# Optimization experiments

Measured on AMD Instinct MI355X. Metric: run time of the kernel, lower is better.

## Reference

```python
import jax, jax.numpy as jnp
import numpy as np

# static sizes (see shape_source)
IN_SIZE = 50000
M = 3            # n_modalities
N0 = 40960       # layer-0 sampled source nodes
N1 = 16384       # layer-0 dst == layer-1 src
B = 4096         # batch (final dst nodes)
HEADS = 4
DIM = 64
HD = HEADS * DIM # 256, integration_size
DEG0, DEG1 = 16, 16
E0, E1 = N1 * DEG0, B * DEG1
NEG_SLOPE = 0.2  # GATConv default negative_slope


def gat_conv(x_src, e_src, e_dst, n_dst, W, att, bias):
    """PyG GATConv with bipartite input (x, None): attention uses only alpha_l.
    x_src: [Ns, HD]; W: [HD, HD]; att: [1, H, C]; returns [n_dst, HD]."""
    x_l = (x_src @ W.T).reshape(-1, HEADS, DIM)            # [Ns, H, C]
    alpha_l = (x_l * att).sum(-1)                          # [Ns, H]
    logits = jax.nn.leaky_relu(alpha_l[e_src], NEG_SLOPE)  # [E, H]
    m = jax.ops.segment_max(logits, e_dst, num_segments=n_dst)
    m = jnp.where(jnp.isfinite(m), m, 0.0)                 # guard empty segments
    e = jnp.exp(logits - m[e_dst])
    denom = jax.ops.segment_sum(e, e_dst, num_segments=n_dst)
    a = e / (denom[e_dst] + 1e-16)                         # edge softmax per dst
    msg = x_l[e_src] * a[:, :, None]                       # [E, H, C]
    out = jax.ops.segment_sum(msg, e_dst, num_segments=n_dst)
    return out.reshape(n_dst, HD) + bias


def interp(scales_param, mask, key):
    """Interp module, evaluate=False, idxs = range(M)."""
    scales = jax.nn.softmax(scales_param, axis=-1)         # [1, M]
    rm = jax.random.randint(key, mask.shape, 0, 2).astype(jnp.float32)
    rm = rm + (1.0 / (1.0 + rm.sum(-1)) ** 20)[:, None]
    rm = rm + (1.0 / (mask.sum(-1) ** 20))[:, None]
    rm = jax.lax.stop_gradient(jnp.floor(rm))              # .int().float()
    rm = rm / (rm + 1e-10)
    m = mask * rm
    m = jax.nn.softmax(m + (1.0 - m) * (-1e10), axis=-1)   # [B, M]
    return scales, m


def setup_inputs() -> dict:
    key = jax.random.key(0)
    ks = jax.random.split(key, 12)
    s = 0.05
    return {
        "masks": jnp.ones((B, M), jnp.float32),
        "n_ids": jax.random.randint(ks[0], (M, N0), 0, IN_SIZE, dtype=jnp.int32),
        "e0_src": jax.random.randint(ks[1], (M, E0), 0, N0, dtype=jnp.int32),
        "e0_dst": jnp.repeat(jnp.arange(N1, dtype=jnp.int32), DEG0),
        "e1_src": jax.random.randint(ks[2], (M, E1), 0, N1, dtype=jnp.int32),
        "e1_dst": jnp.repeat(jnp.arange(B, dtype=jnp.int32), DEG1),
        "pre_W": jax.random.normal(ks[3], (M, HD, IN_SIZE), jnp.float32) * s,
        "pre_b": jax.random.normal(ks[4], (M, HD), jnp.float32) * s,
        "gat_W": jax.random.normal(ks[5], (M, HD, HD), jnp.float32) * s,
        "gat_att": jax.random.normal(ks[6], (M, 1, HEADS, DIM), jnp.float32) * s,
        "gat_b": jax.random.normal(ks[7], (M, HD), jnp.float32) * s,
        "scales_param": jnp.full((1, M), 1.0 / M, jnp.float32),
        "emb_W": jax.random.normal(ks[8], (128, HD), jnp.float32) * s,
        "emb_b": jax.random.normal(ks[9], (128,), jnp.float32) * s,
    }


def reference(masks, n_ids, e0_src, e0_dst, e1_src, e1_dst,
              pre_W, pre_b, gat_W, gat_att, gat_b,
              scales_param, emb_W, emb_b):
    scales, interp_masks = interp(scales_param, masks, jax.random.key(42))
    x_mod = jnp.zeros((B, HD), dtype=masks.dtype)
    for i in range(M):  # small fixed modality loop (structurally distinct params)
        # one-hot(n_id) @ W.T + b  ==  gather of columns of W (same math)
        x = jnp.take(pre_W[i], n_ids[i], axis=1).T + pre_b[i]        # [N0, HD]
        g0 = gat_conv(x, e0_src[i], e0_dst, N1, gat_W[i], gat_att[i], gat_b[i])
        g1 = gat_conv(g0, e1_src[i], e1_dst, B, gat_W[i], gat_att[i], gat_b[i])
        # x_store_layer = [g0[:B] (sliced), g0[:B] (x_pre), g1]; x = sum + g1
        xm = 2.0 * g0[:B] + 2.0 * g1                                  # [B, HD]
        xm = scales[:, i] * interp_masks[:, i].reshape(-1, 1) * xm
        x_mod = x_mod + xm
    emb = x_mod @ emb_W.T + emb_b                                     # [B, 128]
    dot = emb @ emb.T                                                 # [B, B]
    return dot, emb, scales
```

## Files before the change

kernel.cpp:

```cpp
#include <hip/hip_runtime.h>
#include <hip/hip_bf16.h>
#include <cstdint>

#define IN_SZ 50000
#define PADC  50048
#define NM 3
#define N0 40960
#define N1 16384
#define NB 4096
#define HD 256
#define DEG 16
#define E0 (N1*DEG)
#define E1 (NB*DEG)

using short8v = __attribute__((ext_vector_type(8))) short;
using floatx4 = __attribute__((ext_vector_type(4))) float;
typedef unsigned short ushort_t;

__device__ __forceinline__ ushort_t f2bf(float f){
  uint32_t u = __float_as_uint(f);
  uint32_t r = u + 0x7FFFu + ((u>>16)&1u);
  return (ushort_t)(r>>16);
}
__device__ __forceinline__ float bf2f(ushort_t h){
  return __uint_as_float(((uint32_t)h)<<16);
}
__device__ __forceinline__ void gload_lds16(const void* g, void* l){
  __builtin_amdgcn_global_load_lds(
      (const __attribute__((address_space(1))) void*)g,
      (__attribute__((address_space(3))) void*)l, 16, 0, 0);
}

__device__ __forceinline__ uint32_t rotl32(uint32_t x, uint32_t d){ return (x<<d)|(x>>(32u-d)); }

__device__ void tf2x32(uint32_t k0, uint32_t k1, uint32_t c0, uint32_t c1,
                       uint32_t& y0, uint32_t& y1)
{
  uint32_t ks2 = k0 ^ k1 ^ 0x1BD11BDAu;
  uint32_t x0 = c0 + k0, x1 = c1 + k1;
#define R4(a,b,c,d) \
  x0+=x1; x1=rotl32(x1,a); x1^=x0; \
  x0+=x1; x1=rotl32(x1,b); x1^=x0; \
  x0+=x1; x1=rotl32(x1,c); x1^=x0; \
  x0+=x1; x1=rotl32(x1,d); x1^=x0;
  R4(13,15,26,6)  x0+=k1;  x1+=ks2+1u;
  R4(17,29,16,24) x0+=ks2; x1+=k0+2u;
  R4(13,15,26,6)  x0+=k0;  x1+=k1+3u;
  R4(17,29,16,24) x0+=k1;  x1+=ks2+4u;
  R4(13,15,26,6)  x0+=ks2; x1+=k0+5u;
#undef R4
  y0=x0; y1=x1;
}

__global__ __launch_bounds__(256) void prep_k(
    const float* __restrict__ masks, const float* __restrict__ sp,
    float* __restrict__ coef, float* __restrict__ scales_out,
    const float* __restrict__ emb_W, float* __restrict__ wT,
    const float* __restrict__ gat_W, ushort_t* __restrict__ gWhi, ushort_t* __restrict__ gWlo,
    const float* __restrict__ pre_b, const float* __restrict__ gat_att,
    const float* __restrict__ gat_b, float* __restrict__ bsum, float* __restrict__ batt,
    float* __restrict__ watt)
{
  int blk = blockIdx.x;
  int t = threadIdx.x;
  if (blk < 16){
    int b = blk*256 + t;
    float s0=sp[0], s1=sp[1], s2=sp[2];
    float mx = fmaxf(s0,fmaxf(s1,s2));
    float e0=expf(s0-mx), e1=expf(s1-mx), e2=expf(s2-mx);
    float inv = 1.f/(e0+e1+e2);
    float sc[3] = {e0*inv, e1*inv, e2*inv};
    if (b == 0){ scales_out[0]=sc[0]; scales_out[1]=sc[1]; scales_out[2]=sc[2]; }
    uint32_t bits[3];
    uint32_t K0,K1, t0,t1;
    tf2x32(0u,42u,0u,1u,K0,K1);
    for (int i=0;i<3;i++){
      uint32_t idx = (uint32_t)(b*3+i);
      tf2x32(K0,K1,0u,idx,t0,t1);
      bits[i] = (t0 ^ t1) & 1u;
    }
    float mk[3] = {masks[b*3+0], masks[b*3+1], masks[b*3+2]};
    float msum = mk[0]+mk[1]+mk[2];
    float rs = (float)(bits[0]+bits[1]+bits[2]);
    float add = powf(1.f/(1.f+rs), 20.f) + powf(1.f/msum, 20.f);
    float lg[3]; float lmax = -1e30f;
    for (int i=0;i<3;i++){
      float rm = floorf((float)bits[i] + add);
      rm = rm/(rm+1e-10f);
      float mm = mk[i]*rm;
      lg[i] = mm + (1.f-mm)*(-1e10f);
      lmax = fmaxf(lmax, lg[i]);
    }
    float es[3], ssum=0.f;
    for (int i=0;i<3;i++){ es[i]=expf(lg[i]-lmax); ssum+=es[i]; }
    for (int i=0;i<3;i++) coef[b*3+i] = sc[i]*es[i]/ssum;
  } else if (blk < 144){
    int g = (blk-16)*256 + t;
    int j = g >> 8, k = g & 255;
    wT[k*128 + j] = emb_W[g];
  } else if (blk < 912){
    int g = (blk-144)*256 + t;
    float v = gat_W[g];
    ushort_t h = f2bf(v);
    gWhi[g] = h;
    gWlo[g] = f2bf(v - bf2f(h));
  } else if (blk < 915){
    int i = blk - 912, o = t;
    const float* W = gat_W + (size_t)i*HD*HD + (size_t)o*HD;
    const float* b = pre_b + i*HD;
    float s = 0.f;
    for (int k=0;k<HD;k++) s = fmaf(b[k], W[k], s);
    bsum[i*HD + o] = s + gat_b[i*HD + o];
    __shared__ float red[256];
    red[o] = s * gat_att[i*HD + o];
    __syncthreads();
    if (o < 4){
      float p = 0.f;
      for (int j=0;j<64;j++) p += red[o*64 + j];
      batt[i*4 + o] = p;
    }
  } else {
    int idx = blk - 915;
    int i = idx >> 2, h = idx & 3;
    int k = t;
    float s = 0.f;
    for (int o=0;o<64;o++){
      int oo = h*64 + o;
      s = fmaf(gat_W[(size_t)i*HD*HD + (size_t)oo*HD + k], gat_att[i*HD + oo], s);
    }
    watt[(size_t)i*1024 + k*4 + h] = s;
  }
}

__global__ __launch_bounds__(256) void transp4_k(const float* __restrict__ Wb,
                                                 ushort_t* __restrict__ WT_b)
{
  int i = blockIdx.z;
  const float* W = Wb + (size_t)i*HD*IN_SZ;
  ushort_t* WT = WT_b + (size_t)i*(size_t)PADC*HD;
  __shared__ float tile[32][33];
  int c0 = blockIdx.x*32, k0 = blockIdx.y*32;
  int t = threadIdx.x;
  int lk = t>>3, lq = t&7;
  int cbase = c0 + lq*4;
  float4 f;
  if (cbase + 3 < IN_SZ){
    f = *reinterpret_cast<const float4*>(&W[(size_t)(k0+lk)*IN_SZ + cbase]);
  } else {
    float tmp[4] = {0.f,0.f,0.f,0.f};
#pragma unroll
    for (int e=0;e<4;e++) if (cbase+e < IN_SZ) tmp[e] = W[(size_t)(k0+lk)*IN_SZ + cbase+e];
    f = make_float4(tmp[0],tmp[1],tmp[2],tmp[3]);
  }
  tile[lk][lq*4+0]=f.x; tile[lk][lq*4+1]=f.y; tile[lk][lq*4+2]=f.z; tile[lk][lq*4+3]=f.w;
  __syncthreads();
  int sc = t>>3, skq = t&7;
  uint32_t lo = (uint32_t)f2bf(tile[skq*4+0][sc]) | ((uint32_t)f2bf(tile[skq*4+1][sc])<<16);
  uint32_t hi = (uint32_t)f2bf(tile[skq*4+2][sc]) | ((uint32_t)f2bf(tile[skq*4+3][sc])<<16);
  uint2 pack = make_uint2(lo, hi);
  *reinterpret_cast<uint2*>(&WT[(size_t)(c0+sc)*HD + k0 + skq*4]) = pack;
}

__global__ __launch_bounds__(256) void alphaG_k(
    const ushort_t* __restrict__ WT_b, const float* __restrict__ watt_b,
    const float* __restrict__ batt, float* __restrict__ alphaG_b)
{
  int i = blockIdx.y;
  int row0 = blockIdx.x * 64;
  const ushort_t* WT = WT_b + (size_t)i*(size_t)PADC*HD;
  float* alphaG = alphaG_b + (size_t)i*(size_t)PADC*4;
  __shared__ float wl[1024];
  int t = threadIdx.x;
  {
    const float* wg = watt_b + (size_t)i*1024;
#pragma unroll
    for (int j=0;j<4;j++) wl[j*256 + t] = wg[j*256 + t];
  }
  __syncthreads();
  int row = row0 + (t>>2), part = t&3;
  const uint2* rp = reinterpret_cast<const uint2*>(WT + (size_t)row*HD + part*64);
  float p0=0.f,p1=0.f,p2=0.f,p3=0.f;
#pragma unroll
  for (int j=0;j<16;j++){
    uint2 u = rp[j];
    int k = part*64 + 4*j;
    float v0 = bf2f((ushort_t)(u.x & 0xffffu));
    float v1 = bf2f((ushort_t)(u.x >> 16));
    float v2 = bf2f((ushort_t)(u.y & 0xffffu));
    float v3 = bf2f((ushort_t)(u.y >> 16));
    p0 = fmaf(v0, wl[(k+0)*4+0], p0); p1 = fmaf(v0, wl[(k+0)*4+1], p1);
    p2 = fmaf(v0, wl[(k+0)*4+2], p2); p3 = fmaf(v0, wl[(k+0)*4+3], p3);
    p0 = fmaf(v1, wl[(k+1)*4+0], p0); p1 = fmaf(v1, wl[(k+1)*4+1], p1);
    p2 = fmaf(v1, wl[(k+1)*4+2], p2); p3 = fmaf(v1, wl[(k+1)*4+3], p3);
    p0 = fmaf(v2, wl[(k+2)*4+0], p0); p1 = fmaf(v2, wl[(k+2)*4+1], p1);
    p2 = fmaf(v2, wl[(k+2)*4+2], p2); p3 = fmaf(v2, wl[(k+2)*4+3], p3);
    p0 = fmaf(v3, wl[(k+3)*4+0], p0); p1 = fmaf(v3, wl[(k+3)*4+1], p1);
    p2 = fmaf(v3, wl[(k+3)*4+2], p2); p3 = fmaf(v3, wl[(k+3)*4+3], p3);
  }
#pragma unroll
  for (int off=1; off<4; off<<=1){
    p0 += __shfl_xor(p0, off, 64);
    p1 += __shfl_xor(p1, off, 64);
    p2 += __shfl_xor(p2, off, 64);
    p3 += __shfl_xor(p3, off, 64);
  }
  float s = (part==0) ? p0 : (part==1) ? p1 : (part==2) ? p2 : p3;
  s += batt[i*4 + part];
  alphaG[(size_t)row*4 + part] = s > 0.f ? s : 0.2f*s;
}

__global__ __launch_bounds__(128) void gat_msg0w(
    const ushort_t* __restrict__ WT_b, const float* __restrict__ alphaG_b,
    const int* __restrict__ n_ids, const int* __restrict__ esrc_b,
    ushort_t* __restrict__ agg_b)
{
  int i = blockIdx.y, d = blockIdx.x, t = threadIdx.x;
  const ushort_t* WT = WT_b + (size_t)i*(size_t)PADC*HD;
  const float* alphaG = alphaG_b + (size_t)i*(size_t)PADC*4;
  __shared__ int src[16];
  __shared__ float aw[16][4];
  if (t < 16) src[t] = n_ids[(size_t)i*N0 + esrc_b[(size_t)i*E0 + d*16 + t]];
  __syncthreads();
  if (t < 64){
    int e = t&15, h = t>>4;
    float l = alphaG[(size_t)src[e]*4 + h];
    float m = l;
#pragma unroll
    for (int off=1; off<16; off<<=1) m = fmaxf(m, __shfl_xor(m, off, 64));
    float ex = expf(l - m);
    float s = ex;
#pragma unroll
    for (int off=1; off<16; off<<=1) s += __shfl_xor(s, off, 64);
    aw[e][h] = ex / (s + 1e-16f);
  }
  __syncthreads();
  int h = t >> 5;
  float a0=0.f, a1=0.f;
#pragma unroll
  for (int e=0;e<16;e++){
    uint32_t u = *reinterpret_cast<const uint32_t*>(WT + (size_t)src[e]*HD + 2*t);
    float w = aw[e][h];
    a0 = fmaf(w, bf2f((ushort_t)(u & 0xffffu)), a0);
    a1 = fmaf(w, bf2f((ushort_t)(u >> 16)), a1);
  }
  uint32_t pk = (uint32_t)f2bf(a0) | ((uint32_t)f2bf(a1)<<16);
  reinterpret_cast<uint32_t*>(agg_b + ((size_t)i*N1 + d)*HD)[t] = pk;
}

template<bool BIASMODE>
__global__ __launch_bounds__(256) void gemm2(
    const ushort_t* __restrict__ A_b, size_t a_stride,
    const ushort_t* __restrict__ Whi_b, const ushort_t* __restrict__ Wlo_b,
    ushort_t* __restrict__ C_b, size_t c_stride,
    const float* __restrict__ att_b, float* __restrict__ alpha_b, size_t al_stride,
    const float* __restrict__ bias_b)
{
  int i = blockIdx.z;
  int bn0 = blockIdx.x * 128;
  int brow = blockIdx.y * 128;
  const ushort_t* A = A_b + (size_t)i*a_stride;
  const ushort_t* Whi = Whi_b + (size_t)i*HD*HD;
  const ushort_t* Wlo = Wlo_b + (size_t)i*HD*HD;
  ushort_t* C = C_b + (size_t)i*c_stride;

  __shared__ __align__(16) ushort_t smem[2][24*512];
  int t = threadIdx.x, wave = t>>6, lane = t&63;
  int l15 = lane&15, kq = lane>>4;

  int row0 = brow + wave*16 + l15;
  int row1 = brow + (wave+4)*16 + l15;

  const ushort_t* gsrc[6];
  gsrc[0] = A + (size_t)row0*HD + kq*8;
  gsrc[1] = A + (size_t)row1*HD + kq*8;
#pragma unroll
  for (int j=2;j<6;j++){
    int idx = wave + 4*(j-2);
    int ct = idx>>1, h = idx&1;
    const ushort_t* W = h ? Wlo : Whi;
    gsrc[j] = W + (size_t)(bn0 + ct*16 + l15)*HD + kq*8;
  }

  floatx4 acc[4][4];
#pragma unroll
  for (int r=0;r<4;r++)
#pragma unroll
    for (int c=0;c<4;c++) acc[r][c] = (floatx4){0.f,0.f,0.f,0.f};

  int wm = wave>>1, wn = wave&1;

#pragma unroll
  for (int j=0;j<6;j++)
    gload_lds16(gsrc[j], &smem[0][(wave + 4*j)*512] + lane*8);
  __syncthreads();

  for (int cc=0; cc<8; cc++){
    int buf = cc & 1;
    if (cc < 7){
      int k0 = (cc+1)*32;
#pragma unroll
      for (int j=0;j<6;j++)
        gload_lds16(gsrc[j] + k0, &smem[buf^1][(wave + 4*j)*512] + lane*8);
    }
    short8v a[4];
#pragma unroll
    for (int r=0;r<4;r++)
      a[r] = *reinterpret_cast<const short8v*>(&smem[buf][(wm*4+r)*512 + lane*8]);
#pragma unroll
    for (int c=0;c<4;c++){
      int ct = wn*4+c;
      short8v bh = *reinterpret_cast<const short8v*>(&smem[buf][(8+ct*2)*512 + lane*8]);
      short8v bl = *reinterpret_cast<const short8v*>(&smem[buf][(9+ct*2)*512 + lane*8]);
#pragma unroll
      for (int r=0;r<4;r++){
        acc[r][c] = __builtin_amdgcn_mfma_f32_16x16x32_bf16(a[r], bh, acc[r][c], 0,0,0);
        acc[r][c] = __builtin_amdgcn_mfma_f32_16x16x32_bf16(a[r], bl, acc[r][c], 0,0,0);
      }
    }
    __syncthreads();
  }

  float attv[4];
#pragma unroll
  for (int c=0;c<4;c++){
    int col = bn0 + (wn*4+c)*16 + l15;
    if constexpr (BIASMODE) attv[c] = bias_b[i*HD + col];
    else                    attv[c] = att_b[(size_t)i*HD + col];
  }
  int head = (bn0>>6) + wn;
#pragma unroll
  for (int r=0;r<4;r++){
    int rowb = brow + wm*64 + r*16 + kq*4;
#pragma unroll
    for (int j=0;j<4;j++){
      size_t rw = (size_t)(rowb + j)*HD;
#pragma unroll
      for (int c=0;c<4;c++){
        float v = acc[r][c][j];
        if constexpr (BIASMODE) v += attv[c];
        C[rw + bn0 + (wn*4+c)*16 + l15] = f2bf(v);
      }
    }
    if constexpr (!BIASMODE){
#pragma unroll
      for (int j=0;j<4;j++){
        float p = acc[r][0][j]*attv[0] + acc[r][1][j]*attv[1]
                + acc[r][2][j]*attv[2] + acc[r][3][j]*attv[3];
        p += __shfl_xor(p, 1, 64);
        p += __shfl_xor(p, 2, 64);
        p += __shfl_xor(p, 4, 64);
        p += __shfl_xor(p, 8, 64);
        if (l15 == 0){
          float lg = p > 0.f ? p : 0.2f*p;
          alpha_b[(size_t)i*al_stride + (size_t)(rowb + j)*4 + head] = lg;
        }
      }
    }
  }
}

__global__ __launch_bounds__(128) void gat_msg1(
    const ushort_t* __restrict__ xl1hi, const float* __restrict__ alpha1,
    const int* __restrict__ e1src, const float* __restrict__ gat_b,
    const uint32_t* __restrict__ g0_u, const float* __restrict__ coef,
    float* __restrict__ xmod)
{
  int d = blockIdx.x, t = threadIdx.x;
  __shared__ int src[16];
  __shared__ float aw[16][4];
  float o0 = 0.f, o1 = 0.f;
  for (int i=0;i<NM;i++){
    if (t < 16) src[t] = e1src[(size_t)i*E1 + d*16 + t];
    __syncthreads();
    if (t < 64){
      int e = t&15, h = t>>4;
      float l = alpha1[((size_t)i*N1 + src[e])*4 + h];
      float m = l;
#pragma unroll
      for (int off=1; off<16; off<<=1) m = fmaxf(m, __shfl_xor(m, off, 64));
      float ex = expf(l - m);
      float s = ex;
#pragma unroll
      for (int off=1; off<16; off<<=1) s += __shfl_xor(s, off, 64);
      aw[e][h] = ex / (s + 1e-16f);
    }
    __syncthreads();
    const ushort_t* xl = xl1hi + (size_t)i*N1*HD;
    int h = t >> 5;
    float a0=0.f, a1=0.f;
#pragma unroll
    for (int e=0;e<16;e++){
      uint32_t u = *reinterpret_cast<const uint32_t*>(xl + (size_t)src[e]*HD + 2*t);
      float w = aw[e][h];
      a0 = fmaf(w, bf2f((ushort_t)(u & 0xffffu)), a0);
      a1 = fmaf(w, bf2f((ushort_t)(u >> 16)), a1);
    }
    uint32_t gh = g0_u[((size_t)i*N1 + d)*128 + t];
    float g00 = bf2f((ushort_t)(gh & 0xffffu));
    float g01 = bf2f((ushort_t)(gh >> 16));
    const float* bias = gat_b + i*HD;
    float cv = coef[d*3 + i];
    o0 += cv*(2.f*g00 + 2.f*(a0 + bias[2*t]));
    o1 += cv*(2.f*g01 + 2.f*(a1 + bias[2*t+1]));
    __syncthreads();
  }
  *reinterpret_cast<float2*>(&xmod[(size_t)d*HD + 2*t]) = make_float2(o0, o1);
}

__global__ __launch_bounds__(256) void emb_gemm(
  const float* __restrict__ xmod, const float* __restrict__ wT,
  const float* __restrict__ eb, float* __restrict__ emb,
  ushort_t* __restrict__ ehi, ushort_t* __restrict__ elo)
{
  __shared__ float xs[32][260];
  int t = threadIdx.x;
  int brow = blockIdx.x * 32;
#pragma unroll
  for (int j=0;j<8;j++){
    int linear = j*256+t;
    int row = linear >> 6;
    int kq = linear & 63;
    float4 f = *reinterpret_cast<const float4*>(&xmod[(size_t)(brow+row)*256 + kq*4]);
    xs[row][kq*4+0]=f.x; xs[row][kq*4+1]=f.y; xs[row][kq*4+2]=f.z; xs[row][kq*4+3]=f.w;
  }
  __syncthreads();
  int tj = t & 127, th = t >> 7;
  float acc[16];
#pragma unroll
  for(int r=0;r<16;r++) acc[r]=0.f;
  for (int k=0;k<256;k++){
    float w = wT[k*128 + tj];
#pragma unroll
    for (int r=0;r<16;r++) acc[r] = fmaf(xs[th*16+r][k], w, acc[r]);
  }
  float bias = eb[tj];
#pragma unroll
  for (int r=0;r<16;r++){
    size_t idx = (size_t)(brow+th*16+r)*128 + tj;
    float v = acc[r] + bias;
    emb[idx] = v;
    ushort_t hb = f2bf(v);
    ehi[idx] = hb;
    elo[idx] = f2bf(v - bf2f(hb));
  }
}

__global__ __launch_bounds__(256) void dot_mfma(
    const ushort_t* __restrict__ Ehi, const ushort_t* __restrict__ Elo,
    float* __restrict__ dot)
{
  __shared__ __align__(16) ushort_t lb[2][16384];
  int t = threadIdx.x, wave = t>>6, lane = t&63;
  int arow0 = blockIdx.y*128, brow0 = blockIdx.x*128;
  {
    const ushort_t* srcp = (t<128) ? Ehi : Elo;
    ushort_t* dstb = lb[(t<128)?0:1];
    int o = t & 127;
    const ushort_t* rp = srcp + (size_t)(brow0+o)*128;
#pragma unroll
    for (int g=0; g<16; g++){
      short8v v = *reinterpret_cast<const short8v*>(rp + g*8);
      int c = g>>2, grp = g&3;
      int lidx = c*4096 + (o>>4)*512 + ((grp<<4)|(o&15))*8;
      *reinterpret_cast<short8v*>(&dstb[lidx]) = v;
    }
  }
  __syncthreads();

  floatx4 acc[2][8];
#pragma unroll
  for (int rt=0;rt<2;rt++)
#pragma unroll
    for (int ot=0;ot<8;ot++) acc[rt][ot] = (floatx4){0.f,0.f,0.f,0.f};

  int ar0 = arow0 + wave*32 + (lane&15);
  int ar1 = ar0 + 16;
  int koff = (lane>>4)*8;
#pragma unroll
  for (int c=0;c<4;c++){
    short8v ah0 = *reinterpret_cast<const short8v*>(Ehi + (size_t)ar0*128 + c*32 + koff);
    short8v ah1 = *reinterpret_cast<const short8v*>(Ehi + (size_t)ar1*128 + c*32 + koff);
    short8v al0 = *reinterpret_cast<const short8v*>(Elo + (size_t)ar0*128 + c*32 + koff);
    short8v al1 = *reinterpret_cast<const short8v*>(Elo + (size_t)ar1*128 + c*32 + koff);
#pragma unroll
    for (int ot=0;ot<8;ot++){
      short8v bh = *reinterpret_cast<const short8v*>(&lb[0][c*4096 + ot*512 + lane*8]);
      short8v bl = *reinterpret_cast<const short8v*>(&lb[1][c*4096 + ot*512 + lane*8]);
      acc[0][ot] = __builtin_amdgcn_mfma_f32_16x16x32_bf16(ah0, bh, acc[0][ot], 0,0,0);
      acc[0][ot] = __builtin_amdgcn_mfma_f32_16x16x32_bf16(ah0, bl, acc[0][ot], 0,0,0);
      acc[0][ot] = __builtin_amdgcn_mfma_f32_16x16x32_bf16(al0, bh, acc[0][ot], 0,0,0);
      acc[1][ot] = __builtin_amdgcn_mfma_f32_16x16x32_bf16(ah1, bh, acc[1][ot], 0,0,0);
      acc[1][ot] = __builtin_amdgcn_mfma_f32_16x16x32_bf16(ah1, bl, acc[1][ot], 0,0,0);
      acc[1][ot] = __builtin_amdgcn_mfma_f32_16x16x32_bf16(al1, bh, acc[1][ot], 0,0,0);
    }
  }
#pragma unroll
  for (int rt=0;rt<2;rt++){
    int rb = arow0 + wave*32 + rt*16 + (lane>>4)*4;
#pragma unroll
    for (int r=0;r<4;r++)
#pragma unroll
      for (int ot=0;ot<8;ot++)
        dot[(size_t)(rb+r)*4096 + brow0 + ot*16 + (lane&15)] = acc[rt][ot][r];
  }
}

extern "C" void kernel_launch(void* const* d_in, const int* in_sizes, int n_in,
                              void* d_out, int out_size, void* d_ws, size_t ws_size,
                              hipStream_t stream) {
  (void)in_sizes; (void)n_in; (void)out_size; (void)ws_size;
  const float* masks   = (const float*)d_in[0];
  const int*   n_ids   = (const int*)d_in[1];
  const int*   e0_src  = (const int*)d_in[2];
  const int*   e1_src  = (const int*)d_in[4];
  const float* pre_W   = (const float*)d_in[6];
  const float* pre_b   = (const float*)d_in[7];
  const float* gat_W   = (const float*)d_in[8];
  const float* gat_att = (const float*)d_in[9];
  const float* gat_b   = (const float*)d_in[10];
  const float* sp      = (const float*)d_in[11];
  const float* emb_W   = (const float*)d_in[12];
  const float* emb_b   = (const float*)d_in[13];

  float* out = (float*)d_out;
  float* dot = out;
  float* emb = out + (size_t)NB*NB;
  float* scales_out = emb + (size_t)NB*128;

  char* p = (char*)d_ws;
  auto alloc = [&](size_t bytes)->char*{ char* r = p; p += (bytes + 255) & ~(size_t)255; return r; };
  ushort_t* WT    = (ushort_t*)alloc((size_t)NM*PADC*HD*2);
  float*    alphG = (float*)alloc((size_t)NM*PADC*4*4);
  ushort_t* agg   = (ushort_t*)alloc((size_t)NM*N1*HD*2);
  uint32_t* g0u   = (uint32_t*)alloc((size_t)NM*N1*HD*2);
  ushort_t* xl1hi = (ushort_t*)alloc((size_t)NM*N1*HD*2);
  float*    alph1 = (float*)alloc((size_t)NM*N1*4*4);
  float*    xmod  = (float*)alloc((size_t)NB*HD*4);
  float*    coef  = (float*)alloc((size_t)NB*3*4);
  float*    wT    = (float*)alloc((size_t)HD*128*4);
  ushort_t* gWhi  = (ushort_t*)alloc((size_t)NM*HD*HD*2);
  ushort_t* gWlo  = (ushort_t*)alloc((size_t)NM*HD*HD*2);
  float*    bsum  = (float*)alloc((size_t)NM*HD*4);
  float*    batt  = (float*)alloc((size_t)NM*4*4);
  float*    watt  = (float*)alloc((size_t)NM*1024*4);
  ushort_t* ehi   = (ushort_t*)alloc((size_t)NB*128*2);
  ushort_t* elo   = (ushort_t*)alloc((size_t)NB*128*2);

  prep_k<<<927, 256, 0, stream>>>(masks, sp, coef, scales_out, emb_W, wT,
                                  gat_W, gWhi, gWlo, pre_b, gat_att, gat_b,
                                  bsum, batt, watt);
  transp4_k<<<dim3(PADC/32, 8, NM), 256, 0, stream>>>(pre_W, WT);
  alphaG_k<<<dim3(PADC/64, NM), 256, 0, stream>>>(WT, watt, batt, alphG);
  gat_msg0w<<<dim3(N1, NM), 128, 0, stream>>>(WT, alphG, n_ids, e0_src, agg);
  gemm2<true><<<dim3(2, N1/128, NM), 256, 0, stream>>>(
      agg, (size_t)N1*HD, gWhi, gWlo,
      (ushort_t*)g0u, (size_t)N1*HD, nullptr, nullptr, 0, bsum);
  gemm2<false><<<dim3(2, N1/128, NM), 256, 0, stream>>>(
      (const ushort_t*)g0u, (size_t)N1*HD, gWhi, gWlo,
      xl1hi, (size_t)N1*HD, gat_att, alph1, (size_t)N1*4, nullptr);
  gat_msg1<<<NB, 128, 0, stream>>>(xl1hi, alph1, e1_src, gat_b, g0u, coef, xmod);
  emb_gemm<<<NB/32, 256, 0, stream>>>(xmod, wT, emb_b, emb, ehi, elo);
  dot_mfma<<<dim3(32,32), 256, 0, stream>>>(ehi, elo, dot);
}
```

Baseline: 262.0 us.

## Fuse pre_W transpose and attention-logit computation into one kernel

Merges the transpose/bf16 conversion of pre_W and the alphaG logit computation into a single kernel that handles a 64-column by 256-row tile in shared memory. Each thread computes the per-head attention logit from the tile it just converted and writes the transposed row with 16-byte stores. This removes one launch and the re-read of the full bf16 WT buffer (about 77 MB across modalities). In exchange the kernel uses about 37 KB of shared memory per block and holds 32 extra registers per thread, which may lower occupancy.

```diff
diff --git a/kernel.cpp b/kernel.cpp
--- a/kernel.cpp
+++ b/kernel.cpp
@@ -132,43 +132,18 @@
   }
 }
 
-__global__ __launch_bounds__(256) void transp4_k(const float* __restrict__ Wb,
-                                                 ushort_t* __restrict__ WT_b)
-{
-  int i = blockIdx.z;
+__global__ __launch_bounds__(256) void transpA_k(
+    const float* __restrict__ Wb, const float* __restrict__ watt_b,
+    const float* __restrict__ batt, ushort_t* __restrict__ WT_b,
+    float* __restrict__ alphaG_b)
+{
+  int i = blockIdx.y;
+  int c0 = blockIdx.x * 64;
   const float* W = Wb + (size_t)i*HD*IN_SZ;
   ushort_t* WT = WT_b + (size_t)i*(size_t)PADC*HD;
-  __shared__ float tile[32][33];
-  int c0 = blockIdx.x*32, k0 = blockIdx.y*32;
-  int t = threadIdx.x;
-  int lk = t>>3, lq = t&7;
-  int cbase = c0 + lq*4;
-  float4 f;
-  if (cbase + 3 < IN_SZ){
-    f = *reinterpret_cast<const float4*>(&W[(size_t)(k0+lk)*IN_SZ + cbase]);
-  } else {
-    float tmp[4] = {0.f,0.f,0.f,0.f};
-#pragma unroll
-    for (int e=0;e<4;e++) if (cbase+e < IN_SZ) tmp[e] = W[(size_t)(k0+lk)*IN_SZ + cbase+e];
-    f = make_float4(tmp[0],tmp[1],tmp[2],tmp[3]);
-  }
-  tile[lk][lq*4+0]=f.x; tile[lk][lq*4+1]=f.y; tile[lk][lq*4+2]=f.z; tile[lk][lq*4+3]=f.w;
-  __syncthreads();
-  int sc = t>>3, skq = t&7;
-  uint32_t lo = (uint32_t)f2bf(tile[skq*4+0][sc]) | ((uint32_t)f2bf(tile[skq*4+1][sc])<<16);
-  uint32_t hi = (uint32_t)f2bf(tile[skq*4+2][sc]) | ((uint32_t)f2bf(tile[skq*4+3][sc])<<16);
-  uint2 pack = make_uint2(lo, hi);
-  *reinterpret_cast<uint2*>(&WT[(size_t)(c0+sc)*HD + k0 + skq*4]) = pack;
-}
-
-__global__ __launch_bounds__(256) void alphaG_k(
-    const ushort_t* __restrict__ WT_b, const float* __restrict__ watt_b,
-    const float* __restrict__ batt, float* __restrict__ alphaG_b)
-{
-  int i = blockIdx.y;
-  int row0 = blockIdx.x * 64;
-  const ushort_t* WT = WT_b + (size_t)i*(size_t)PADC*HD;
   float* alphaG = alphaG_b + (size_t)i*(size_t)PADC*4;
+
+  __shared__ uint32_t tile[256*33];
   __shared__ float wl[1024];
   int t = threadIdx.x;
   {
@@ -176,37 +151,55 @@
 #pragma unroll
     for (int j=0;j<4;j++) wl[j*256 + t] = wg[j*256 + t];
   }
+#pragma unroll
+  for (int it=0; it<16; it++){
+    int lin = it*256 + t;
+    int k = lin >> 4, quad = lin & 15;
+    int cb = c0 + quad*4;
+    float4 f;
+    if (cb + 3 < IN_SZ){
+      f = *reinterpret_cast<const float4*>(&W[(size_t)k*IN_SZ + cb]);
+    } else {
+      float tmp[4] = {0.f,0.f,0.f,0.f};
+#pragma unroll
+      for (int e=0;e<4;e++) if (cb+e < IN_SZ) tmp[e] = W[(size_t)k*IN_SZ + cb+e];
+      f = make_float4(tmp[0],tmp[1],tmp[2],tmp[3]);
+    }
+    tile[k*33 + quad*2]     = (uint32_t)f2bf(f.x) | ((uint32_t)f2bf(f.y)<<16);
+    tile[k*33 + quad*2 + 1] = (uint32_t)f2bf(f.z) | ((uint32_t)f2bf(f.w)<<16);
+  }
   __syncthreads();
-  int row = row0 + (t>>2), part = t&3;
-  const uint2* rp = reinterpret_cast<const uint2*>(WT + (size_t)row*HD + part*64);
+
+  int c = t>>2, kp = t&3, half = c&1, cu = c>>1;
   float p0=0.f,p1=0.f,p2=0.f,p3=0.f;
-#pragma unroll
-  for (int j=0;j<16;j++){
-    uint2 u = rp[j];
-    int k = part*64 + 4*j;
-    float v0 = bf2f((ushort_t)(u.x & 0xffffu));
-    float v1 = bf2f((ushort_t)(u.x >> 16));
-    float v2 = bf2f((ushort_t)(u.y & 0xffffu));
-    float v3 = bf2f((ushort_t)(u.y >> 16));
-    p0 = fmaf(v0, wl[(k+0)*4+0], p0); p1 = fmaf(v0, wl[(k+0)*4+1], p1);
-    p2 = fmaf(v0, wl[(k+0)*4+2], p2); p3 = fmaf(v0, wl[(k+0)*4+3], p3);
-    p0 = fmaf(v1, wl[(k+1)*4+0], p0); p1 = fmaf(v1, wl[(k+1)*4+1], p1);
-    p2 = fmaf(v1, wl[(k+1)*4+2], p2); p3 = fmaf(v1, wl[(k+1)*4+3], p3);
-    p0 = fmaf(v2, wl[(k+2)*4+0], p0); p1 = fmaf(v2, wl[(k+2)*4+1], p1);
-    p2 = fmaf(v2, wl[(k+2)*4+2], p2); p3 = fmaf(v2, wl[(k+2)*4+3], p3);
-    p0 = fmaf(v3, wl[(k+3)*4+0], p0); p1 = fmaf(v3, wl[(k+3)*4+1], p1);
-    p2 = fmaf(v3, wl[(k+3)*4+2], p2); p3 = fmaf(v3, wl[(k+3)*4+3], p3);
-  }
-#pragma unroll
-  for (int off=1; off<4; off<<=1){
-    p0 += __shfl_xor(p0, off, 64);
-    p1 += __shfl_xor(p1, off, 64);
-    p2 += __shfl_xor(p2, off, 64);
-    p3 += __shfl_xor(p3, off, 64);
-  }
-  float s = (part==0) ? p0 : (part==1) ? p1 : (part==2) ? p2 : p3;
-  s += batt[i*4 + part];
-  alphaG[(size_t)row*4 + part] = s > 0.f ? s : 0.2f*s;
+  uint32_t ou[32];
+#pragma unroll
+  for (int j=0;j<32;j++){
+    int k0 = kp*64 + 2*j;
+    uint32_t ua = tile[k0*33 + cu];
+    uint32_t ub = tile[(k0+1)*33 + cu];
+    ushort_t va = half ? (ushort_t)(ua>>16) : (ushort_t)(ua & 0xffffu);
+    ushort_t vb = half ? (ushort_t)(ub>>16) : (ushort_t)(ub & 0xffffu);
+    ou[j] = (uint32_t)va | ((uint32_t)vb<<16);
+    float fa = bf2f(va), fb = bf2f(vb);
+    p0 = fmaf(fa, wl[k0*4+0], p0); p1 = fmaf(fa, wl[k0*4+1], p1);
+    p2 = fmaf(fa, wl[k0*4+2], p2); p3 = fmaf(fa, wl[k0*4+3], p3);
+    p0 = fmaf(fb, wl[(k0+1)*4+0], p0); p1 = fmaf(fb, wl[(k0+1)*4+1], p1);
+    p2 = fmaf(fb, wl[(k0+1)*4+2], p2); p3 = fmaf(fb, wl[(k0+1)*4+3], p3);
+  }
+  uint32_t* orow = reinterpret_cast<uint32_t*>(WT + (size_t)(c0+c)*HD + kp*64);
+#pragma unroll
+  for (int j=0;j<8;j++){
+    uint4 v = make_uint4(ou[4*j], ou[4*j+1], ou[4*j+2], ou[4*j+3]);
+    *reinterpret_cast<uint4*>(orow + j*4) = v;
+  }
+  p0 += __shfl_xor(p0, 1, 64); p0 += __shfl_xor(p0, 2, 64);
+  p1 += __shfl_xor(p1, 1, 64); p1 += __shfl_xor(p1, 2, 64);
+  p2 += __shfl_xor(p2, 1, 64); p2 += __shfl_xor(p2, 2, 64);
+  p3 += __shfl_xor(p3, 1, 64); p3 += __shfl_xor(p3, 2, 64);
+  float pv = (kp==0) ? p0 : (kp==1) ? p1 : (kp==2) ? p2 : p3;
+  pv += batt[i*4 + kp];
+  alphaG[(size_t)(c0+c)*4 + kp] = pv > 0.f ? pv : 0.2f*pv;
 }
 
 __global__ __launch_bounds__(128) void gat_msg0w(
@@ -549,8 +542,7 @@
   prep_k<<<927, 256, 0, stream>>>(masks, sp, coef, scales_out, emb_W, wT,
                                   gat_W, gWhi, gWlo, pre_b, gat_att, gat_b,
                                   bsum, batt, watt);
-  transp4_k<<<dim3(PADC/32, 8, NM), 256, 0, stream>>>(pre_W, WT);
-  alphaG_k<<<dim3(PADC/64, NM), 256, 0, stream>>>(WT, watt, batt, alphG);
+  transpA_k<<<dim3(PADC/64, NM), 256, 0, stream>>>(pre_W, watt, batt, WT, alphG);
   gat_msg0w<<<dim3(N1, NM), 128, 0, stream>>>(WT, alphG, n_ids, e0_src, agg);
   gemm2<true><<<dim3(2, N1/128, NM), 256, 0, stream>>>(
       agg, (size_t)N1*HD, gWhi, gWlo,
```

Measured after the change: 274.7 us. 4.9% more time.
